# Performance work log

Measured on AMD Instinct MI355X. Metric: run time of the kernel, lower is better.

## Reference

```python
import jax, jax.numpy as jnp
import numpy as np

B, S, D, H = 4, 2048, 1024, 16
HD = D // H  # head_dim = 64


def setup_inputs() -> dict:
    key = jax.random.key(0)
    kx, kq, kk, kv, ko = jax.random.split(key, 5)
    scale = 1.0 / np.sqrt(D)
    return {
        "x": jax.random.normal(kx, (B, S, D), dtype=jnp.float32),
        "wq": jax.random.normal(kq, (D, D), dtype=jnp.float32) * scale,
        "wk": jax.random.normal(kk, (D, D), dtype=jnp.float32) * scale,
        "wv": jax.random.normal(kv, (D, D), dtype=jnp.float32) * scale,
        "wo": jax.random.normal(ko, (D, D), dtype=jnp.float32) * scale,
    }


def reference(x, wq, wk, wv, wo):
    b, s, d = x.shape
    # nn.Linear stores weight [out, in]: y = x @ W.T
    q = (x @ wq.T).reshape(b, s, H, HD)
    k = (x @ wk.T).reshape(b, s, H, HD)
    v = (x @ wv.T).reshape(b, s, H, HD)
    # scores: [b, h, s, s]
    scores = jnp.einsum("bqhd,bkhd->bhqk", q, k) / np.sqrt(HD)
    causal = jnp.triu(jnp.ones((s, s), dtype=bool), k=1)
    scores = jnp.where(causal, -jnp.inf, scores)
    attn = jax.nn.softmax(scores, axis=-1)
    out = jnp.einsum("bhqk,bkhd->bqhd", attn, v).reshape(b, s, d)
    return out @ wo.T
```

## Files before the change

### kernel.cpp

```cpp
#include <hip/hip_runtime.h>
#include <math.h>

typedef unsigned short u16;
typedef __attribute__((ext_vector_type(8))) short short8;
typedef __attribute__((ext_vector_type(4))) short short4v;
typedef __attribute__((ext_vector_type(4))) float f32x4;
typedef __attribute__((ext_vector_type(2))) unsigned int uint2v;

constexpr int Bn = 4, Sn = 2048, Dn = 1024, Hn = 16;
constexpr float SCL = 0.125f * 1.44269504f;

__device__ __forceinline__ u16 f2bf(float f) {
  unsigned u = __float_as_uint(f);
  u += 0x7fffu + ((u >> 16) & 1u);
  return (u16)(u >> 16);
}

__device__ __forceinline__ f32x4 mfma32(short8 a, short8 b, f32x4 c) {
  return __builtin_amdgcn_mfma_f32_16x16x32_bf16(a, b, c, 0, 0, 0);
}

__device__ __forceinline__ f32x4 mfma16(short4v a, short4v b, f32x4 c) {
#if __has_builtin(__builtin_amdgcn_mfma_f32_16x16x16_bf16)
  return __builtin_amdgcn_mfma_f32_16x16x16_bf16(a, b, c, 0, 0, 0);
#elif __has_builtin(__builtin_amdgcn_mfma_f32_16x16x16bf16_1k)
  return __builtin_amdgcn_mfma_f32_16x16x16bf16_1k(a, b, c, 0, 0, 0);
#else
  short8 a8 = {a[0], a[1], a[2], a[3], 0, 0, 0, 0};
  short8 b8 = {b[0], b[1], b[2], b[3], 0, 0, 0, 0};
  return __builtin_amdgcn_mfma_f32_16x16x32_bf16(a8, b8, c, 0, 0, 0);
#endif
}

__device__ __forceinline__ void gl_lds16(const u16* g, u16* l) {
  __builtin_amdgcn_global_load_lds(
      (const __attribute__((address_space(1))) unsigned int*)g,
      (__attribute__((address_space(3))) unsigned int*)l, 16, 0, 0);
}

__global__ __launch_bounds__(256) void cast_all(
    const float4* __restrict__ x, const float4* __restrict__ wq,
    const float4* __restrict__ wk, const float4* __restrict__ wv,
    const float4* __restrict__ wo, ushort4* __restrict__ xb,
    ushort4* __restrict__ wqb, ushort4* __restrict__ wkb,
    ushort4* __restrict__ wvb, ushort4* __restrict__ wob) {
  const int blk = blockIdx.x;
  const float4* in;
  ushort4* out;
  int base;
  float s = 1.0f;
  if (blk < 8192) {
    in = x; out = xb; base = blk;
  } else if (blk < 9216) {
    in = wq; out = wqb; base = blk - 8192; s = SCL;
  } else if (blk < 10240) {
    in = wk; out = wkb; base = blk - 9216;
  } else if (blk < 11264) {
    in = wv; out = wvb; base = blk - 10240;
  } else {
    in = wo; out = wob; base = blk - 11264;
  }
  const int i = base * 256 + threadIdx.x;
  const float4 f = in[i];
  ushort4 o;
  o.x = f2bf(f.x * s); o.y = f2bf(f.y * s);
  o.z = f2bf(f.z * s); o.w = f2bf(f.w * s);
  out[i] = o;
}

template <int MODE>
__device__ __forceinline__ void gemm_body(const u16* __restrict__ A,
                                          const u16* __restrict__ W,
                                          u16* __restrict__ Cb,
                                          float* __restrict__ Cf,
                                          int bx, int by,
                                          u16* __restrict__ Asm,
                                          u16* __restrict__ Wsm) {
  const int t = threadIdx.x;
  const int w = t >> 6, l = t & 63;
  const int wy = w >> 1, wx = w & 1;
  const int q = l >> 4, r = l & 15;
  const int m0 = bx * 128, n0 = by * 128;

  f32x4 acc[4][4] = {};

  for (int k0 = 0; k0 < 1024; k0 += 64) {
    __syncthreads();
#pragma unroll
    for (int i = 0; i < 4; ++i) {
      const int c = t + i * 256;
      const int row = c >> 3, cl = c & 7;
      const int cg = cl ^ (row & 7);
      gl_lds16(A + (size_t)(m0 + row) * 1024 + k0 + cg * 8, &Asm[c * 8]);
      gl_lds16(W + (size_t)(n0 + row) * 1024 + k0 + cg * 8, &Wsm[c * 8]);
    }
    __syncthreads();
#pragma unroll
    for (int kf = 0; kf < 2; ++kf) {
      short8 af[4], bf[4];
#pragma unroll
      for (int mi = 0; mi < 4; ++mi) {
        const int rowA = wy * 64 + mi * 16 + r;
        af[mi] = *(const short8*)&Asm[rowA * 64 + ((kf * 4 + q) ^ (rowA & 7)) * 8];
        const int rowB = wx * 64 + mi * 16 + r;
        bf[mi] = *(const short8*)&Wsm[rowB * 64 + ((kf * 4 + q) ^ (rowB & 7)) * 8];
      }
#pragma unroll
      for (int mi = 0; mi < 4; ++mi)
#pragma unroll
        for (int ni = 0; ni < 4; ++ni)
          acc[mi][ni] = mfma32(af[mi], bf[ni], acc[mi][ni]);
    }
  }

  if (MODE == 2) {
    const int bq = m0 >> 11;
    const int jt = ((m0 & 2047) >> 6) + wy;
    const int hh = (n0 >> 6) + wx;
    u16* vt_t = Cb + ((size_t)((bq * 16 + hh) * 32) + jt) * 4096;
#pragma unroll
    for (int mi = 0; mi < 4; ++mi)
#pragma unroll
      for (int ni = 0; ni < 4; ++ni) {
        short4v pk;
#pragma unroll
        for (int e = 0; e < 4; ++e) pk[e] = (short)f2bf(acc[mi][ni][e]);
        const int hd = ni * 16 + r;
        const int c2 = q + 4 * (mi >> 1);
        *(short4v*)&vt_t[hd * 64 + ((c2 ^ (r & 7)) * 8) + (mi & 1) * 4] = pk;
      }
    return;
  }

#pragma unroll
  for (int mi = 0; mi < 4; ++mi) {
    const int row = m0 + wy * 64 + mi * 16 + q * 4;
#pragma unroll
    for (int ni = 0; ni < 4; ++ni) {
      const int col = n0 + wx * 64 + ni * 16 + r;
#pragma unroll
      for (int e = 0; e < 4; ++e) {
        if (MODE == 1)
          Cf[(size_t)(row + e) * 1024 + col] = acc[mi][ni][e];
        else
          Cb[(size_t)(row + e) * 1024 + col] = f2bf(acc[mi][ni][e]);
      }
    }
  }
}

__global__ __launch_bounds__(256) void gemm_qkv(const u16* __restrict__ A,
                                                const u16* __restrict__ Wq,
                                                const u16* __restrict__ Wk,
                                                const u16* __restrict__ Wv,
                                                u16* __restrict__ Cq,
                                                u16* __restrict__ Ck,
                                                u16* __restrict__ Vt) {
  __shared__ u16 Asm[128 * 64];
  __shared__ u16 Wsm[128 * 64];
  const int z = blockIdx.z;
  if (z == 2)
    gemm_body<2>(A, Wv, Vt, nullptr, blockIdx.x, blockIdx.y, Asm, Wsm);
  else
    gemm_body<0>(A, z ? Wk : Wq, z ? Ck : Cq, nullptr, blockIdx.x, blockIdx.y,
                 Asm, Wsm);
}

__global__ __launch_bounds__(256) void gemm_out(const u16* __restrict__ A,
                                                const u16* __restrict__ W,
                                                float* __restrict__ C) {
  __shared__ u16 Asm[128 * 64];
  __shared__ u16 Wsm[128 * 64];
  gemm_body<1>(A, W, nullptr, C, blockIdx.x, blockIdx.y, Asm, Wsm);
}

__global__ __launch_bounds__(128) void attn_v9(const u16* __restrict__ Qb,
                                               const u16* __restrict__ Kb,
                                               const u16* __restrict__ Vt,
                                               u16* __restrict__ Ob) {
  const int i = blockIdx.x;
  const int st = 31 - (i >> 6);
  const int grp = (i & 7) + 8 * ((i >> 3) & 7);
  const int b = grp >> 4, h = grp & 15;
  const int t = threadIdx.x;
  const int w = t >> 6, l = t & 63;
  const int q = l >> 4, r = l & 15;

  __shared__ u16 Kd[2][4096];
  __shared__ u16 Vd[2][4096];

  const size_t kgbase = (size_t)(b * Sn) * Dn + h * 64;
  const size_t vgbase = (size_t)((b * Hn + h) * 32) * 4096;

  const u16* kg[4];
  const u16* vg[4];
#pragma unroll
  for (int ii = 0; ii < 4; ++ii) {
    const int c = t + ii * 128, row = c >> 3, cl = c & 7;
    kg[ii] = Kb + kgbase + (size_t)row * Dn + (cl ^ (row & 7)) * 8;
    vg[ii] = Vt + vgbase + c * 8;
  }
  const int rx = r & 7;
  const int b0 = r * 64 + ((q ^ rx) * 8);
  const int b1 = r * 64 + (((4 + q) ^ rx) * 8);

  const int qb64 = st * 64;

  short8 Qf[2][2];
#pragma unroll
  for (int mi = 0; mi < 2; ++mi)
#pragma unroll
    for (int kf = 0; kf < 2; ++kf)
      Qf[mi][kf] = *(const short8*)(Qb +
          (size_t)(b * Sn + qb64 + w * 32 + mi * 16 + r) * Dn + h * 64 +
          kf * 32 + q * 8);

  f32x4 O[2][4] = {};
  float l_[2] = {0.f, 0.f};

#pragma unroll
  for (int ii = 0; ii < 4; ++ii) {
    const int c8 = (t + ii * 128) * 8;
    gl_lds16(kg[ii], &Kd[0][c8]);
    gl_lds16(vg[ii], &Vd[0][c8]);
  }
  const u16* kgt[4];
  const u16* vgt[4];
#pragma unroll
  for (int ii = 0; ii < 4; ++ii) {
    kgt[ii] = kg[ii] + 64 * Dn;
    vgt[ii] = vg[ii] + 4096;
  }

  for (int jt = 0; jt <= st; ++jt) {
    __syncthreads();
    if (jt < st) {
      u16* kl = &Kd[(jt + 1) & 1][0];
      u16* vl = &Vd[(jt + 1) & 1][0];
#pragma unroll
      for (int ii = 0; ii < 4; ++ii) {
        const int c8 = (t + ii * 128) * 8;
        gl_lds16(kgt[ii], kl + c8);
        gl_lds16(vgt[ii], vl + c8);
        kgt[ii] += 64 * Dn;
        vgt[ii] += 4096;
      }
    }
    const u16* KtA = &Kd[jt & 1][b0];
    const u16* KtB = &Kd[jt & 1][b1];

    short8 Kf[4][2];
#pragma unroll
    for (int ni = 0; ni < 4; ++ni) {
      Kf[ni][0] = *(const short8*)(KtA + ni * 1024);
      Kf[ni][1] = *(const short8*)(KtB + ni * 1024);
    }

    f32x4 S[2][4] = {};
    __builtin_amdgcn_s_setprio(1);
#pragma unroll
    for (int ni = 0; ni < 4; ++ni)
#pragma unroll
      for (int kf = 0; kf < 2; ++kf) {
        S[0][ni] = mfma32(Kf[ni][kf], Qf[0][kf], S[0][ni]);
        S[1][ni] = mfma32(Kf[ni][kf], Qf[1][kf], S[1][ni]);
      }
    __builtin_amdgcn_s_setprio(0);

    if (jt == st) {
#pragma unroll
      for (int mi = 0; mi < 2; ++mi) {
        const int qrow = w * 32 + mi * 16 + r;
#pragma unroll
        for (int ni = 0; ni < 4; ++ni) {
          const int key = ni * 16 + q * 4;
#pragma unroll
          for (int e = 0; e < 4; ++e)
            if (key + e > qrow) S[mi][ni][e] = -3.0e38f;
        }
      }
    }

    short4v Pf[2][4];
#pragma unroll
    for (int mi = 0; mi < 2; ++mi)
#pragma unroll
      for (int ni = 0; ni < 4; ++ni) {
        const float p0 = __builtin_amdgcn_exp2f(S[mi][ni][0]);
        const float p1 = __builtin_amdgcn_exp2f(S[mi][ni][1]);
        const float p2 = __builtin_amdgcn_exp2f(S[mi][ni][2]);
        const float p3 = __builtin_amdgcn_exp2f(S[mi][ni][3]);
        l_[mi] += (p0 + p1) + (p2 + p3);
        unsigned plo, phi;
        asm("v_cvt_pk_bf16_f32 %0, %1, %2" : "=v"(plo) : "v"(p0), "v"(p1));
        asm("v_cvt_pk_bf16_f32 %0, %1, %2" : "=v"(phi) : "v"(p2), "v"(p3));
        const uint2v pk2 = {plo, phi};
        Pf[mi][ni] = __builtin_bit_cast(short4v, pk2);
      }

    const u16* VsA = &Vd[jt & 1][b0];
    const u16* VsB = &Vd[jt & 1][b1];
    __builtin_amdgcn_s_setprio(1);
#pragma unroll
    for (int np = 0; np < 2; ++np)
#pragma unroll
      for (int ni2 = 0; ni2 < 4; ++ni2) {
        const short8 vv =
            *(const short8*)((np ? VsB : VsA) + ni2 * 1024);
        const short4v va = {vv[0], vv[1], vv[2], vv[3]};
        const short4v vb2 = {vv[4], vv[5], vv[6], vv[7]};
        O[0][ni2] = mfma16(va, Pf[0][2 * np], O[0][ni2]);
        O[0][ni2] = mfma16(vb2, Pf[0][2 * np + 1], O[0][ni2]);
        O[1][ni2] = mfma16(va, Pf[1][2 * np], O[1][ni2]);
        O[1][ni2] = mfma16(vb2, Pf[1][2 * np + 1], O[1][ni2]);
      }
    __builtin_amdgcn_s_setprio(0);
  }

#pragma unroll
  for (int mi = 0; mi < 2; ++mi) {
    float s = l_[mi];
    s += __shfl_xor(s, 16, 64);
    s += __shfl_xor(s, 32, 64);
    const float rl = __builtin_amdgcn_rcpf(s);
#pragma unroll
    for (int ni2 = 0; ni2 < 4; ++ni2) {
      short4v o;
#pragma unroll
      for (int e = 0; e < 4; ++e) o[e] = (short)f2bf(O[mi][ni2][e] * rl);
      *(short4v*)(Ob + (size_t)(b * Sn + qb64 + w * 32 + mi * 16 + r) * Dn +
                  h * 64 + ni2 * 16 + q * 4) = o;
    }
  }
}

extern "C" void kernel_launch(void* const* d_in, const int* in_sizes, int n_in,
                              void* d_out, int out_size, void* d_ws, size_t ws_size,
                              hipStream_t stream) {
  const float* x  = (const float*)d_in[0];
  const float* wq = (const float*)d_in[1];
  const float* wk = (const float*)d_in[2];
  const float* wv = (const float*)d_in[3];
  const float* wo = (const float*)d_in[4];
  float* out = (float*)d_out;

  u16* xb  = (u16*)d_ws;
  u16* wqb = xb + 8388608;
  u16* wkb = wqb + 1048576;
  u16* wvb = wkb + 1048576;
  u16* wob = wvb + 1048576;
  u16* qb  = wob + 1048576;
  u16* kb  = qb + 8388608;
  u16* vt2 = kb + 8388608;
  u16* aob = vt2 + 8388608;

  cast_all<<<12288, 256, 0, stream>>>(
      (const float4*)x, (const float4*)wq, (const float4*)wk,
      (const float4*)wv, (const float4*)wo, (ushort4*)xb, (ushort4*)wqb,
      (ushort4*)wkb, (ushort4*)wvb, (ushort4*)wob);

  gemm_qkv<<<dim3(64, 8, 3), 256, 0, stream>>>(xb, wqb, wkb, wvb, qb, kb, vt2);

  attn_v9<<<2048, 128, 0, stream>>>(qb, kb, vt2, aob);

  gemm_out<<<dim3(64, 8), 256, 0, stream>>>(aob, wob, out);
}
```

Before: 240.8 us.

## Single-buffer V tile loaded in-iteration and use 16x16x32 MFMA for PV

The attention kernel now single-buffers the V tile in LDS. Each iteration issues the V load for the current tile and waits on it with an explicit vmcnt and barrier just before the PV product, so the load overlaps the QK^T and softmax work. The PV product packs probabilities into 8-wide bf16 fragments and uses the 16x16x32 MFMA, halving the PV MFMA count. This shrinks LDS use and instruction count. The cost is that V load latency is only hidden behind one tile of compute, and correctness now depends on hand-counted vmcnt values.

```diff
diff --git a/kernel.cpp b/kernel.cpp
--- a/kernel.cpp
+++ b/kernel.cpp
@@ -6,6 +6,7 @@
 typedef __attribute__((ext_vector_type(4))) short short4v;
 typedef __attribute__((ext_vector_type(4))) float f32x4;
 typedef __attribute__((ext_vector_type(2))) unsigned int uint2v;
+typedef __attribute__((ext_vector_type(4))) unsigned int uint4v;
 
 constexpr int Bn = 4, Sn = 2048, Dn = 1024, Hn = 16;
 constexpr float SCL = 0.125f * 1.44269504f;
@@ -18,18 +19,6 @@
 
 __device__ __forceinline__ f32x4 mfma32(short8 a, short8 b, f32x4 c) {
   return __builtin_amdgcn_mfma_f32_16x16x32_bf16(a, b, c, 0, 0, 0);
-}
-
-__device__ __forceinline__ f32x4 mfma16(short4v a, short4v b, f32x4 c) {
-#if __has_builtin(__builtin_amdgcn_mfma_f32_16x16x16_bf16)
-  return __builtin_amdgcn_mfma_f32_16x16x16_bf16(a, b, c, 0, 0, 0);
-#elif __has_builtin(__builtin_amdgcn_mfma_f32_16x16x16bf16_1k)
-  return __builtin_amdgcn_mfma_f32_16x16x16bf16_1k(a, b, c, 0, 0, 0);
-#else
-  short8 a8 = {a[0], a[1], a[2], a[3], 0, 0, 0, 0};
-  short8 b8 = {b[0], b[1], b[2], b[3], 0, 0, 0, 0};
-  return __builtin_amdgcn_mfma_f32_16x16x32_bf16(a8, b8, c, 0, 0, 0);
-#endif
 }
 
 __device__ __forceinline__ void gl_lds16(const u16* g, u16* l) {
@@ -174,10 +163,10 @@
   gemm_body<1>(A, W, nullptr, C, blockIdx.x, blockIdx.y, Asm, Wsm);
 }
 
-__global__ __launch_bounds__(128) void attn_v9(const u16* __restrict__ Qb,
-                                               const u16* __restrict__ Kb,
-                                               const u16* __restrict__ Vt,
-                                               u16* __restrict__ Ob) {
+__global__ __launch_bounds__(128) void attn_v10(const u16* __restrict__ Qb,
+                                                const u16* __restrict__ Kb,
+                                                const u16* __restrict__ Vt,
+                                                u16* __restrict__ Ob) {
   const int i = blockIdx.x;
   const int st = 31 - (i >> 6);
   const int grp = (i & 7) + 8 * ((i >> 3) & 7);
@@ -187,7 +176,7 @@
   const int q = l >> 4, r = l & 15;
 
   __shared__ u16 Kd[2][4096];
-  __shared__ u16 Vd[2][4096];
+  __shared__ u16 Vd[4096];
 
   const size_t kgbase = (size_t)(b * Sn) * Dn + h * 64;
   const size_t vgbase = (size_t)((b * Hn + h) * 32) * 4096;
@@ -219,33 +208,34 @@
   float l_[2] = {0.f, 0.f};
 
 #pragma unroll
-  for (int ii = 0; ii < 4; ++ii) {
-    const int c8 = (t + ii * 128) * 8;
-    gl_lds16(kg[ii], &Kd[0][c8]);
-    gl_lds16(vg[ii], &Vd[0][c8]);
-  }
+  for (int ii = 0; ii < 4; ++ii)
+    gl_lds16(kg[ii], &Kd[0][(t + ii * 128) * 8]);
+
   const u16* kgt[4];
   const u16* vgt[4];
 #pragma unroll
   for (int ii = 0; ii < 4; ++ii) {
     kgt[ii] = kg[ii] + 64 * Dn;
-    vgt[ii] = vg[ii] + 4096;
+    vgt[ii] = vg[ii];
   }
 
   for (int jt = 0; jt <= st; ++jt) {
     __syncthreads();
+
+#pragma unroll
+    for (int ii = 0; ii < 4; ++ii) {
+      gl_lds16(vgt[ii], &Vd[(t + ii * 128) * 8]);
+      vgt[ii] += 4096;
+    }
     if (jt < st) {
       u16* kl = &Kd[(jt + 1) & 1][0];
-      u16* vl = &Vd[(jt + 1) & 1][0];
 #pragma unroll
       for (int ii = 0; ii < 4; ++ii) {
-        const int c8 = (t + ii * 128) * 8;
-        gl_lds16(kgt[ii], kl + c8);
-        gl_lds16(vgt[ii], vl + c8);
+        gl_lds16(kgt[ii], kl + (t + ii * 128) * 8);
         kgt[ii] += 64 * Dn;
-        vgt[ii] += 4096;
-      }
-    }
+      }
+    }
+
     const u16* KtA = &Kd[jt & 1][b0];
     const u16* KtB = &Kd[jt & 1][b1];
 
@@ -281,39 +271,48 @@
       }
     }
 
-    short4v Pf[2][4];
+    short8 P8[2][2];
 #pragma unroll
     for (int mi = 0; mi < 2; ++mi)
 #pragma unroll
-      for (int ni = 0; ni < 4; ++ni) {
-        const float p0 = __builtin_amdgcn_exp2f(S[mi][ni][0]);
-        const float p1 = __builtin_amdgcn_exp2f(S[mi][ni][1]);
-        const float p2 = __builtin_amdgcn_exp2f(S[mi][ni][2]);
-        const float p3 = __builtin_amdgcn_exp2f(S[mi][ni][3]);
-        l_[mi] += (p0 + p1) + (p2 + p3);
-        unsigned plo, phi;
-        asm("v_cvt_pk_bf16_f32 %0, %1, %2" : "=v"(plo) : "v"(p0), "v"(p1));
-        asm("v_cvt_pk_bf16_f32 %0, %1, %2" : "=v"(phi) : "v"(p2), "v"(p3));
-        const uint2v pk2 = {plo, phi};
-        Pf[mi][ni] = __builtin_bit_cast(short4v, pk2);
-      }
-
-    const u16* VsA = &Vd[jt & 1][b0];
-    const u16* VsB = &Vd[jt & 1][b1];
+      for (int np = 0; np < 2; ++np) {
+        unsigned pw[4];
+#pragma unroll
+        for (int half = 0; half < 2; ++half) {
+          const int ni = 2 * np + half;
+          const float p0 = __builtin_amdgcn_exp2f(S[mi][ni][0]);
+          const float p1 = __builtin_amdgcn_exp2f(S[mi][ni][1]);
+          const float p2 = __builtin_amdgcn_exp2f(S[mi][ni][2]);
+          const float p3 = __builtin_amdgcn_exp2f(S[mi][ni][3]);
+          l_[mi] += (p0 + p1) + (p2 + p3);
+          unsigned plo, phi;
+          asm("v_cvt_pk_bf16_f32 %0, %1, %2" : "=v"(plo) : "v"(p0), "v"(p1));
+          asm("v_cvt_pk_bf16_f32 %0, %1, %2" : "=v"(phi) : "v"(p2), "v"(p3));
+          pw[half * 2] = plo;
+          pw[half * 2 + 1] = phi;
+        }
+        const uint4v pk4 = {pw[0], pw[1], pw[2], pw[3]};
+        P8[mi][np] = __builtin_bit_cast(short8, pk4);
+      }
+
+    if (jt < st)
+      asm volatile("s_waitcnt vmcnt(4)" ::: "memory");
+    else
+      asm volatile("s_waitcnt vmcnt(0)" ::: "memory");
+    __builtin_amdgcn_s_barrier();
+    __builtin_amdgcn_sched_barrier(0);
+
     __builtin_amdgcn_s_setprio(1);
 #pragma unroll
-    for (int np = 0; np < 2; ++np)
+    for (int np = 0; np < 2; ++np) {
+      const int vb = np ? b1 : b0;
 #pragma unroll
       for (int ni2 = 0; ni2 < 4; ++ni2) {
-        const short8 vv =
-            *(const short8*)((np ? VsB : VsA) + ni2 * 1024);
-        const short4v va = {vv[0], vv[1], vv[2], vv[3]};
-        const short4v vb2 = {vv[4], vv[5], vv[6], vv[7]};
-        O[0][ni2] = mfma16(va, Pf[0][2 * np], O[0][ni2]);
-        O[0][ni2] = mfma16(vb2, Pf[0][2 * np + 1], O[0][ni2]);
-        O[1][ni2] = mfma16(va, Pf[1][2 * np], O[1][ni2]);
-        O[1][ni2] = mfma16(vb2, Pf[1][2 * np + 1], O[1][ni2]);
-      }
+        const short8 vvx = *(const short8*)(&Vd[vb + ni2 * 1024]);
+        O[0][ni2] = mfma32(vvx, P8[0][np], O[0][ni2]);
+        O[1][ni2] = mfma32(vvx, P8[1][np], O[1][ni2]);
+      }
+    }
     __builtin_amdgcn_s_setprio(0);
   }
 
@@ -361,7 +360,7 @@
 
   gemm_qkv<<<dim3(64, 8, 3), 256, 0, stream>>>(xb, wqb, wkb, wvb, qb, kb, vt2);
 
-  attn_v9<<<2048, 128, 0, stream>>>(qb, kb, vt2, aob);
+  attn_v10<<<2048, 128, 0, stream>>>(qb, kb, vt2, aob);
 
   gemm_out<<<dim3(64, 8), 256, 0, stream>>>(aob, wob, out);
 }
```

After: 220.4 us. 8.5% less time.
